# Kernel optimization log

Hardware: AMD Instinct MI355X
Metric: run time of the kernel (lower is better)

## Reference

```python
import jax, jax.numpy as jnp
import numpy as np

B, C, V, L = 32, 32, 1024, 13  # batch, channels, nodes, seq_len
SUPPORT_LEN, ORDER = 3, 2
C_IN_TOTAL = (ORDER * SUPPORT_LEN + 1) * C  # 224
C_OUT = 64


def setup_inputs() -> dict:
    key = jax.random.key(0)
    ks = jax.random.split(key, 6)
    x = jax.random.normal(ks[0], (B, C, V, L), dtype=jnp.float32)
    # row-normalized random adjacencies (dense diffusion matrices)
    def adj(k):
        a = jax.random.uniform(k, (V, V), dtype=jnp.float32)
        return a / jnp.sum(a, axis=1, keepdims=True)
    A0, A1, A2 = adj(ks[1]), adj(ks[2]), adj(ks[3])
    W = jax.random.normal(ks[4], (C_OUT, C_IN_TOTAL), dtype=jnp.float32) * (1.0 / np.sqrt(C_IN_TOTAL))
    b = jnp.zeros((C_OUT,), dtype=jnp.float32)
    return {"x": x, "A0": A0, "A1": A1, "A2": A2, "W": W, "b": b}


def nconv(x, A):
    # x: [b, c, v, l], A: [v, w] -> [b, c, w, l]
    return jnp.einsum('bcvl,vw->bcwl', x, A)


def reference(x, A0, A1, A2, W, b):
    out = [x]
    for A in (A0, A1, A2):
        x1 = nconv(x, A)
        out.append(x1)
        for _ in range(2, ORDER + 1):
            x2 = nconv(x1, A)
            out.append(x2)
            x1 = x2
    h = jnp.concatenate(out, axis=1)  # [b, (order*support_len+1)*c, v, l]
    # 1x1 conv == channel contraction; dropout is identity in eval mode
    return jnp.einsum('bcvl,oc->bovl', h, W) + b[None, :, None, None]
```

## Files before the change

### kernel.cpp

```cpp
#include <hip/hip_runtime.h>
#include <hip/hip_bf16.h>
#include <cstdint>


#define SZE 13631488ull
#define OFF_AT  190840832ull
#define OFF_WB  197132288ull
#define WS_NEED 197160960ull

typedef __attribute__((ext_vector_type(8))) short short8;
typedef __attribute__((ext_vector_type(4))) float f32x4;

__device__ __forceinline__ unsigned short f2b(float f) {
    unsigned int u = __builtin_bit_cast(unsigned int, f);
    u += 0x7FFFu + ((u >> 16) & 1u);
    return (unsigned short)(u >> 16);
}

__device__ __forceinline__ void gl2lds16(const unsigned short* g, unsigned short* l) {
    __builtin_amdgcn_global_load_lds(
        (__attribute__((address_space(1))) void*)(g),
        (__attribute__((address_space(3))) void*)(l), 16, 0, 0);
}

__global__ __launch_bounds__(256) void k_prep(const float* __restrict__ x,
                                              unsigned short* __restrict__ T,
                                              unsigned short* __restrict__ Ht) {
    __shared__ unsigned short sb[32 * 840];
    const int b = blockIdx.x >> 4, vc = blockIdx.x & 15;
    const int t = threadIdx.x;
    const float4* xb = (const float4*)x;
    for (int it = 0; it < 26; ++it) {
        int q = it * 256 + t;
        int c = q / 208, f = q - c * 208;
        float4 u = xb[(size_t)(b * 32 + c) * 3328 + vc * 208 + f];
        ushort4 pk; pk.x = f2b(u.x); pk.y = f2b(u.y); pk.z = f2b(u.z); pk.w = f2b(u.w);
        *(ushort4*)(sb + c * 840 + f * 4) = pk;
    }
    __syncthreads();
    unsigned short* Tb = T + (size_t)b * 13 * 32 * 1024 + (size_t)vc * 64;
    for (int it = 0; it < 26; ++it) {
        int q = it * 256 + t;
        int l = q >> 9, r = q & 511, c = r >> 4, sg = r & 15;
        const unsigned short* src = sb + c * 840 + l;
        ushort4 pk;
        pk.x = src[(sg * 4 + 0) * 13];
        pk.y = src[(sg * 4 + 1) * 13];
        pk.z = src[(sg * 4 + 2) * 13];
        pk.w = src[(sg * 4 + 3) * 13];
        *(ushort4*)(Tb + (size_t)(l * 32 + c) * 1024 + sg * 4) = pk;
    }
    unsigned short* Hb = Ht + ((size_t)b * 13312 + (size_t)vc * 832) * 224;
    for (int it = 0; it < 26; ++it) {
        int q = it * 256 + t;
        int v = q / 104, r = q - v * 104, l = r >> 3, cs = r & 7;
        const unsigned short* src = sb + v * 13 + l;
        ushort4 pk;
        pk.x = src[(cs * 4 + 0) * 840];
        pk.y = src[(cs * 4 + 1) * 840];
        pk.z = src[(cs * 4 + 2) * 840];
        pk.w = src[(cs * 4 + 3) * 840];
        *(ushort4*)(Hb + (size_t)(v * 13 + l) * 224 + cs * 4) = pk;
    }
}

__global__ __launch_bounds__(256) void k_prep_A(const float* __restrict__ A0,
                                                const float* __restrict__ A1,
                                                const float* __restrict__ A2,
                                                unsigned short* __restrict__ AT,
                                                unsigned short* __restrict__ Abf) {
    const float* A = blockIdx.z == 0 ? A0 : blockIdx.z == 1 ? A1 : A2;
    unsigned short* D = AT + (size_t)blockIdx.z * 1024 * 1024;
    unsigned short* D2 = Abf + (size_t)blockIdx.z * 1024 * 1024;
    __shared__ float tile[32][33];
    int v0 = blockIdx.y * 32, w0 = blockIdx.x * 32;
    int c = threadIdx.x & 31, r = threadIdx.x >> 5;
    for (int p = 0; p < 4; ++p) {
        int rr = r + p * 8;
        float val = A[(size_t)(v0 + rr) * 1024 + w0 + c];
        tile[rr][c] = val;
        D2[(size_t)(v0 + rr) * 1024 + w0 + c] = f2b(val);
    }
    __syncthreads();
    for (int p = 0; p < 4; ++p) {
        int rr = r + p * 8;
        D[(size_t)(w0 + rr) * 1024 + v0 + c] = f2b(tile[c][rr]);
    }
}

__global__ __launch_bounds__(256) void k_prep_W(const float* __restrict__ W,
                                                unsigned short* __restrict__ Wb) {
    int idx = blockIdx.x * 256 + threadIdx.x;
    Wb[idx] = f2b(W[idx]);
}

__global__ __launch_bounds__(256) void k_gemm(const unsigned short* __restrict__ Xb, long xz,
                                              const unsigned short* __restrict__ P0,
                                              const unsigned short* __restrict__ P1,
                                              unsigned short* __restrict__ Tout, long tz,
                                              unsigned short* __restrict__ Ht, int doT) {
    __shared__ union {
        struct { unsigned short xs[8192]; unsigned short ps[8192]; } s;
        unsigned short cs[128 * 132];
        unsigned short ct[128 * 136];
    } lds;
    const int z = blockIdx.z;
    const unsigned short* X = Xb + (size_t)z * (size_t)xz;
    const unsigned short* P = (z < 3) ? P0 + (size_t)z * 1048576u
                                      : P1 + (size_t)(z - 3) * 1048576u;
    const int i0 = blockIdx.x * 128;
    const int j0 = blockIdx.y * 128;
    const int t = threadIdx.x;
    const int lane = t & 63, wave = t >> 6;
    const int l16 = lane & 15, quad = lane >> 4;
    const int wi = (wave >> 1) * 64, wj = (wave & 1) * 64;

    f32x4 acc[4][4] = {};

    const int row = t >> 2, seg = t & 3;
    const unsigned short* xg0 = X + (size_t)(i0 + row) * 1024 + seg * 8;
    const unsigned short* xg1 = xg0 + (size_t)64 * 1024;
    const unsigned short* pg0 = P + (size_t)(j0 + row) * 1024 + seg * 8;
    const unsigned short* pg1 = pg0 + (size_t)64 * 1024;
    unsigned short* lx0 = lds.s.xs + t * 8;
    unsigned short* lp0 = lds.s.ps + t * 8;

    for (int kt = 0; kt < 16; ++kt) {
        const int ko = kt * 64;
        gl2lds16(xg0 + ko,      lx0);
        gl2lds16(xg1 + ko,      lx0 + 2048);
        gl2lds16(xg0 + ko + 32, lx0 + 4096);
        gl2lds16(xg1 + ko + 32, lx0 + 6144);
        gl2lds16(pg0 + ko,      lp0);
        gl2lds16(pg1 + ko,      lp0 + 2048);
        gl2lds16(pg0 + ko + 32, lp0 + 4096);
        gl2lds16(pg1 + ko + 32, lp0 + 6144);
        __syncthreads();
#pragma unroll
        for (int p = 0; p < 2; ++p) {
            short8 a[4], b[4];
#pragma unroll
            for (int mi = 0; mi < 4; ++mi)
                a[mi] = *(const short8*)(lds.s.xs + p * 4096 + (wi + mi * 16 + l16) * 32 + quad * 8);
#pragma unroll
            for (int nj = 0; nj < 4; ++nj)
                b[nj] = *(const short8*)(lds.s.ps + p * 4096 + (wj + nj * 16 + l16) * 32 + quad * 8);
#pragma unroll
            for (int mi = 0; mi < 4; ++mi)
#pragma unroll
                for (int nj = 0; nj < 4; ++nj)
                    acc[mi][nj] = __builtin_amdgcn_mfma_f32_16x16x32_bf16(a[mi], b[nj], acc[mi][nj], 0, 0, 0);
        }
        __syncthreads();
    }

    if (doT) {
#pragma unroll
        for (int mi = 0; mi < 4; ++mi)
#pragma unroll
            for (int nj = 0; nj < 4; ++nj)
#pragma unroll
                for (int r = 0; r < 4; ++r)
                    lds.cs[(wi + mi * 16 + quad * 4 + r) * 132 + (wj + nj * 16 + l16)] =
                        f2b(acc[mi][nj][r]);
        __syncthreads();
        unsigned short* O = Tout + (size_t)z * (size_t)tz;
#pragma unroll
        for (int rep = 0; rep < 8; ++rep) {
            int q = rep * 256 + t;
            int rr = q >> 4, sg = q & 15;
            *(uint4*)(O + (size_t)(i0 + rr) * 1024 + j0 + sg * 8) =
                *(const uint4*)(lds.cs + rr * 132 + sg * 8);
        }
        __syncthreads();
    }

    if (Ht) {
#pragma unroll
        for (int mi = 0; mi < 4; ++mi)
#pragma unroll
            for (int nj = 0; nj < 4; ++nj) {
                ushort4 pk;
                pk.x = f2b(acc[mi][nj][0]);
                pk.y = f2b(acc[mi][nj][1]);
                pk.z = f2b(acc[mi][nj][2]);
                pk.w = f2b(acc[mi][nj][3]);
                *(ushort4*)(lds.ct + (wj + nj * 16 + l16) * 136 + wi + mi * 16 + quad * 4) = pk;
            }
        __syncthreads();
        const int cc0 = (z < 3) ? 32 + 64 * z : 64 * (z - 2);
#pragma unroll
        for (int it = 0; it < 8; ++it) {
            int q = it * 256 + t;
            int sg = q & 3, v = (q >> 2) & 127, s = q >> 9;
            int p = (i0 >> 5) + s;
            int b = p / 13, l = p - b * 13;
            size_t m = (size_t)b * 13312 + (size_t)(j0 + v) * 13 + l;
            *(uint4*)(Ht + m * 224 + cc0 + sg * 8) =
                *(const uint4*)(lds.ct + v * 136 + s * 32 + sg * 8);
        }
    }
}

__global__ __launch_bounds__(128) void k_fc(const unsigned short* __restrict__ Ht,
                                            const unsigned short* __restrict__ Wb,
                                            const float* __restrict__ bias,
                                            float* __restrict__ y) {
    __shared__ unsigned short sw[64 * 232];
    const int bid = blockIdx.x;
    const int b = bid >> 5, v0 = (bid & 31) * 32;
    const int t = threadIdx.x;
    const int lane = t & 63, wave = t >> 6;
    const int l16 = lane & 15, quad = lane >> 4;

    for (int it = 0; it < 14; ++it) {
        int q = it * 128 + t;
        int o = q / 28, sg = q % 28;
        *(uint4*)(sw + o * 232 + sg * 8) = *(const uint4*)(Wb + o * 224 + sg * 8);
    }

    const size_t mw = (size_t)b * 13312 + (size_t)v0 * 13 + wave * 208;
    const unsigned short* ag = Ht + (mw + l16) * 224 + quad * 8;
    float* yb = y + (size_t)b * 851968 + (size_t)v0 * 13 + wave * 208 + quad * 4;

    float bv[4];
#pragma unroll
    for (int nj = 0; nj < 4; ++nj) bv[nj] = bias[nj * 16 + l16];

    short8 cur[7];
#pragma unroll
    for (int kk = 0; kk < 7; ++kk)
        cur[kk] = *(const short8*)(ag + kk * 32);
    __syncthreads();

#pragma unroll 1
    for (int mf = 0; mf < 13; ++mf) {
        const int mfn = (mf < 12) ? mf + 1 : 0;
        short8 nxt[7];
#pragma unroll
        for (int kk = 0; kk < 7; ++kk)
            nxt[kk] = *(const short8*)(ag + (size_t)mfn * 3584 + kk * 32);
        f32x4 acc[4];
#pragma unroll
        for (int nj = 0; nj < 4; ++nj) acc[nj] = (f32x4){bv[nj], bv[nj], bv[nj], bv[nj]};
#pragma unroll
        for (int kk = 0; kk < 7; ++kk)
#pragma unroll
            for (int nj = 0; nj < 4; ++nj) {
                short8 bf = *(const short8*)(sw + (nj * 16 + l16) * 232 + kk * 32 + quad * 8);
                acc[nj] = __builtin_amdgcn_mfma_f32_16x16x32_bf16(cur[kk], bf, acc[nj], 0, 0, 0);
            }
#pragma unroll
        for (int nj = 0; nj < 4; ++nj)
            *(f32x4*)(yb + (size_t)(nj * 16 + l16) * 13312 + mf * 16) = acc[nj];
#pragma unroll
        for (int kk = 0; kk < 7; ++kk) cur[kk] = nxt[kk];
    }
}

extern "C" void kernel_launch(void* const* d_in, const int* in_sizes, int n_in,
                              void* d_out, int out_size, void* d_ws, size_t ws_size,
                              hipStream_t stream) {
    const float* x    = (const float*)d_in[0];
    const float* A0   = (const float*)d_in[1];
    const float* A1   = (const float*)d_in[2];
    const float* A2   = (const float*)d_in[3];
    const float* W    = (const float*)d_in[4];
    const float* bias = (const float*)d_in[5];

    if (ws_size < WS_NEED) return;

    unsigned short* Ht = (unsigned short*)d_ws;
    unsigned short* AT = (unsigned short*)((char*)d_ws + OFF_AT);
    unsigned short* Wb = (unsigned short*)((char*)d_ws + OFF_WB);
    unsigned short* Tarena = (unsigned short*)d_out;
    unsigned short* Abf = Tarena + SZE;
    unsigned short* AT2 = Tarena + 2 * SZE;

    k_prep<<<512, 256, 0, stream>>>(x, Tarena, Ht);
    k_prep_A<<<dim3(32, 32, 3), 256, 0, stream>>>(A0, A1, A2, AT, Abf);
    k_prep_W<<<56, 256, 0, stream>>>(W, Wb);
    k_gemm<<<dim3(8, 8, 3), 256, 0, stream>>>(AT, 1048576L, Abf, Abf,
                                              AT2, 1048576L, nullptr, 1);
    k_gemm<<<dim3(104, 8, 6), 256, 0, stream>>>(Tarena, 0L, AT, AT2,
                                                nullptr, 0L, Ht, 0);
    k_fc<<<1024, 128, 0, stream>>>(Ht, Wb, bias, (float*)d_out);
}
```

Measured before the change: 468.9 us.

## Replace main diffusion GEMM with 256x256-tile pipelined MFMA kernel

Adds a new 512-thread GEMM kernel with 256x256 output tiles. It prefetches K-chunks into double-buffered LDS through direct global-to-LDS loads with explicit vmcnt/lgkmcnt waits, barriers and priority bumps around MFMA bursts. It also drops the LDS-transposed epilogue for Ht and writes accumulators straight to the scattered Ht layout. The intent is more data reuse per tile and overlap of loads with MFMA work. The trade-offs are a 128KB LDS footprint, more registers, and less coalesced 8-byte epilogue stores.

```diff
diff --git a/kernel.cpp b/kernel.cpp
--- a/kernel.cpp
+++ b/kernel.cpp
@@ -102,7 +102,6 @@
     __shared__ union {
         struct { unsigned short xs[8192]; unsigned short ps[8192]; } s;
         unsigned short cs[128 * 132];
-        unsigned short ct[128 * 136];
     } lds;
     const int z = blockIdx.z;
     const unsigned short* X = Xb + (size_t)z * (size_t)xz;
@@ -172,32 +171,148 @@
             *(uint4*)(O + (size_t)(i0 + rr) * 1024 + j0 + sg * 8) =
                 *(const uint4*)(lds.cs + rr * 132 + sg * 8);
         }
-        __syncthreads();
-    }
-
-    if (Ht) {
-#pragma unroll
-        for (int mi = 0; mi < 4; ++mi)
-#pragma unroll
-            for (int nj = 0; nj < 4; ++nj) {
-                ushort4 pk;
-                pk.x = f2b(acc[mi][nj][0]);
-                pk.y = f2b(acc[mi][nj][1]);
-                pk.z = f2b(acc[mi][nj][2]);
-                pk.w = f2b(acc[mi][nj][3]);
-                *(ushort4*)(lds.ct + (wj + nj * 16 + l16) * 136 + wi + mi * 16 + quad * 4) = pk;
-            }
-        __syncthreads();
-        const int cc0 = (z < 3) ? 32 + 64 * z : 64 * (z - 2);
-#pragma unroll
-        for (int it = 0; it < 8; ++it) {
-            int q = it * 256 + t;
-            int sg = q & 3, v = (q >> 2) & 127, s = q >> 9;
-            int p = (i0 >> 5) + s;
-            int b = p / 13, l = p - b * 13;
-            size_t m = (size_t)b * 13312 + (size_t)(j0 + v) * 13 + l;
-            *(uint4*)(Ht + m * 224 + cc0 + sg * 8) =
-                *(const uint4*)(lds.ct + v * 136 + s * 32 + sg * 8);
+    }
+}
+
+__global__ __launch_bounds__(512, 2) void k_gemm256(
+        const unsigned short* __restrict__ Xb,
+        const unsigned short* __restrict__ P0,
+        const unsigned short* __restrict__ P1,
+        unsigned short* __restrict__ Ht) {
+    __shared__ unsigned short lds[65536];
+    const int z = blockIdx.z;
+    const unsigned short* P = (z < 3) ? P0 + (size_t)z * 1048576u
+                                      : P1 + (size_t)(z - 3) * 1048576u;
+    const int i0 = blockIdx.x * 256;
+    const int j0 = blockIdx.y * 256;
+    const int t = threadIdx.x;
+    const int lane = t & 63;
+    const int l16 = lane & 15, quad = lane >> 4;
+    const int wave = t >> 6, wm = wave >> 2, wn = wave & 3;
+
+    const unsigned short* pa0 = Xb + (size_t)(i0 + (t >> 2)) * 1024 + (t & 3) * 8;
+    const unsigned short* pb0 = P  + (size_t)(j0 + (t >> 2)) * 1024 + (t & 3) * 8;
+
+    const int aoff = (wm * 128 + l16) * 32 + quad * 8;
+    const int boff = 16384 + (wn * 64 + l16) * 32 + quad * 8;
+
+    auto stage = [&](int H) {
+        if (H >= 64) return;
+        const int kt = H >> 2, h = H & 3;
+        const int ks = h >> 1;
+        const unsigned short* s = ((h & 1) ? pb0 : pa0) + kt * 64 + ks * 32;
+        unsigned short* d = lds + (kt & 1) * 32768 + (h & 1) * 16384 + ks * 8192 + t * 8;
+        gl2lds16(s, d);
+        gl2lds16(s + 131072, d + 4096);
+    };
+
+    f32x4 acc[8][4] = {};
+
+#pragma unroll
+    for (int H = 0; H < 7; ++H) stage(H);
+    asm volatile("s_waitcnt vmcnt(6)" ::: "memory");
+    __builtin_amdgcn_s_barrier();
+
+#pragma unroll 1
+    for (int kt = 0; kt < 16; ++kt) {
+        const int base = (kt & 1) * 32768;
+        const int P4 = kt * 4;
+        short8 a[8], b0, b1;
+
+#pragma unroll
+        for (int mi = 0; mi < 8; ++mi)
+            a[mi] = *(const short8*)(lds + base + aoff + mi * 512);
+        b0 = *(const short8*)(lds + base + boff);
+        b1 = *(const short8*)(lds + base + boff + 512);
+        stage(P4 + 7);
+        __builtin_amdgcn_sched_barrier(0);
+        __builtin_amdgcn_s_barrier();
+        asm volatile("s_waitcnt lgkmcnt(0)" ::: "memory");
+        __builtin_amdgcn_sched_barrier(0);
+        __builtin_amdgcn_s_setprio(1);
+#pragma unroll
+        for (int mi = 0; mi < 8; ++mi) {
+            acc[mi][0] = __builtin_amdgcn_mfma_f32_16x16x32_bf16(a[mi], b0, acc[mi][0], 0, 0, 0);
+            acc[mi][1] = __builtin_amdgcn_mfma_f32_16x16x32_bf16(a[mi], b1, acc[mi][1], 0, 0, 0);
+        }
+        __builtin_amdgcn_s_setprio(0);
+        __builtin_amdgcn_sched_barrier(0);
+        __builtin_amdgcn_s_barrier();
+
+        b0 = *(const short8*)(lds + base + boff + 2 * 512);
+        b1 = *(const short8*)(lds + base + boff + 3 * 512);
+        stage(P4 + 8);
+        __builtin_amdgcn_sched_barrier(0);
+        __builtin_amdgcn_s_barrier();
+        asm volatile("s_waitcnt lgkmcnt(0)" ::: "memory");
+        __builtin_amdgcn_sched_barrier(0);
+        __builtin_amdgcn_s_setprio(1);
+#pragma unroll
+        for (int mi = 0; mi < 8; ++mi) {
+            acc[mi][2] = __builtin_amdgcn_mfma_f32_16x16x32_bf16(a[mi], b0, acc[mi][2], 0, 0, 0);
+            acc[mi][3] = __builtin_amdgcn_mfma_f32_16x16x32_bf16(a[mi], b1, acc[mi][3], 0, 0, 0);
+        }
+        __builtin_amdgcn_s_setprio(0);
+        __builtin_amdgcn_sched_barrier(0);
+        __builtin_amdgcn_s_barrier();
+
+#pragma unroll
+        for (int mi = 0; mi < 8; ++mi)
+            a[mi] = *(const short8*)(lds + base + 8192 + aoff + mi * 512);
+        b0 = *(const short8*)(lds + base + 8192 + boff);
+        b1 = *(const short8*)(lds + base + 8192 + boff + 512);
+        stage(P4 + 9);
+        __builtin_amdgcn_sched_barrier(0);
+        __builtin_amdgcn_s_barrier();
+        asm volatile("s_waitcnt lgkmcnt(0)" ::: "memory");
+        __builtin_amdgcn_sched_barrier(0);
+        __builtin_amdgcn_s_setprio(1);
+#pragma unroll
+        for (int mi = 0; mi < 8; ++mi) {
+            acc[mi][0] = __builtin_amdgcn_mfma_f32_16x16x32_bf16(a[mi], b0, acc[mi][0], 0, 0, 0);
+            acc[mi][1] = __builtin_amdgcn_mfma_f32_16x16x32_bf16(a[mi], b1, acc[mi][1], 0, 0, 0);
+        }
+        __builtin_amdgcn_s_setprio(0);
+        __builtin_amdgcn_sched_barrier(0);
+        __builtin_amdgcn_s_barrier();
+
+        b0 = *(const short8*)(lds + base + 8192 + boff + 2 * 512);
+        b1 = *(const short8*)(lds + base + 8192 + boff + 3 * 512);
+        stage(P4 + 10);
+        if (kt < 14)      asm volatile("s_waitcnt vmcnt(6)" ::: "memory");
+        else if (kt == 14) asm volatile("s_waitcnt vmcnt(0)" ::: "memory");
+        __builtin_amdgcn_sched_barrier(0);
+        __builtin_amdgcn_s_barrier();
+        asm volatile("s_waitcnt lgkmcnt(0)" ::: "memory");
+        __builtin_amdgcn_sched_barrier(0);
+        __builtin_amdgcn_s_setprio(1);
+#pragma unroll
+        for (int mi = 0; mi < 8; ++mi) {
+            acc[mi][2] = __builtin_amdgcn_mfma_f32_16x16x32_bf16(a[mi], b0, acc[mi][2], 0, 0, 0);
+            acc[mi][3] = __builtin_amdgcn_mfma_f32_16x16x32_bf16(a[mi], b1, acc[mi][3], 0, 0, 0);
+        }
+        __builtin_amdgcn_s_setprio(0);
+        __builtin_amdgcn_sched_barrier(0);
+        __builtin_amdgcn_s_barrier();
+    }
+
+    const int cc0 = (z < 3) ? 32 + 64 * z : 64 * (z - 2);
+    const int wc = j0 + wn * 64 + l16;
+#pragma unroll
+    for (int mi = 0; mi < 8; ++mi) {
+        int p = (i0 >> 5) + wm * 4 + (mi >> 1);
+        int b = p / 13, l = p - b * 13;
+        int cc = cc0 + (mi & 1) * 16 + quad * 4;
+#pragma unroll
+        for (int nj = 0; nj < 4; ++nj) {
+            int w = wc + nj * 16;
+            size_t m = (size_t)b * 13312 + (size_t)w * 13 + l;
+            ushort4 pk;
+            pk.x = f2b(acc[mi][nj][0]);
+            pk.y = f2b(acc[mi][nj][1]);
+            pk.z = f2b(acc[mi][nj][2]);
+            pk.w = f2b(acc[mi][nj][3]);
+            *(ushort4*)(Ht + m * 224 + cc) = pk;
         }
     }
 }
@@ -282,7 +397,6 @@
     k_prep_W<<<56, 256, 0, stream>>>(W, Wb);
     k_gemm<<<dim3(8, 8, 3), 256, 0, stream>>>(AT, 1048576L, Abf, Abf,
                                               AT2, 1048576L, nullptr, 1);
-    k_gemm<<<dim3(104, 8, 6), 256, 0, stream>>>(Tarena, 0L, AT, AT2,
-                                                nullptr, 0L, Ht, 0);
+    k_gemm256<<<dim3(52, 4, 6), 512, 0, stream>>>(Tarena, AT, AT2, Ht);
     k_fc<<<1024, 128, 0, stream>>>(Ht, Wb, bias, (float*)d_out);
 }
```

Result: slower. 484.7 us (+3.4%).
